# Kernel tuning notes

Measured on AMD Instinct MI355X. Metric: run time of the kernel, lower is better.

The kernel has to match this reference:

```python
import jax, jax.numpy as jnp
import numpy as np

N = 1024
IN_CH = 128
EDGE_CH = 32
OUT_CH = 128


def setup_inputs() -> dict:
    key = jax.random.key(0)
    ks = jax.random.split(key, 8)
    return {
        "node_mat": jax.random.normal(ks[0], (N, IN_CH), dtype=jnp.float32),
        "adj": jax.random.uniform(ks[1], (N, N), dtype=jnp.float32),
        "edge_adj": jax.random.uniform(ks[2], (EDGE_CH, N, N), dtype=jnp.float32),
        "node_weight": jax.random.normal(ks[3], (IN_CH, OUT_CH), dtype=jnp.float32) * 0.05,
        "edge_lay_1": jax.random.normal(ks[4], (EDGE_CH, OUT_CH - 1), dtype=jnp.float32) * 0.05,
        "edge_lay_2": jax.random.normal(ks[5], (OUT_CH - 1, OUT_CH), dtype=jnp.float32) * 0.05,
        "root": jax.random.normal(ks[6], (IN_CH, OUT_CH), dtype=jnp.float32) * 0.05,
        "bias": jax.random.normal(ks[7], (OUT_CH,), dtype=jnp.float32) * 0.05,
    }


def reference(node_mat, adj, edge_adj, node_weight, edge_lay_1, edge_lay_2, root, bias):
    # node message passing: adj-weighted sum of transformed node features  [N, out]
    sum_filter_node_msgs = adj @ (node_mat @ node_weight)
    # edge MLP: 2-layer with ReLU, applied over the edge-channel axis
    # edge_adj: [E, N, N]; edge_lay_1: [E, out-1] -> h1: [out-1, N, N]
    h1 = jnp.maximum(jnp.einsum('enm,eb->bnm', edge_adj, edge_lay_1), 0.0)
    # h1: [out-1, N, N]; edge_lay_2: [out-1, out] -> h2: [out, N, N]
    h2 = jnp.einsum('bnm,bo->onm', h1, edge_lay_2)
    # adjacency-weighted compression: e_compress[n, o] = sum_m h2[o, n, m] * adj[n, m]
    e_compress = jnp.einsum('onm,nm->no', h2, adj)
    root_info = node_mat @ root
    return sum_filter_node_msgs + e_compress + root_info + bias
```

## Files before the change

### kernel.cpp

```cpp
#include <hip/hip_runtime.h>
#include <hip/hip_bf16.h>

#define NN 1024
#define IN_CH 128
#define EDGE_CH 32
#define OUT_CH 128

typedef __attribute__((ext_vector_type(8))) short bf16x8;
typedef __attribute__((ext_vector_type(4))) float f32x4;

static __device__ __forceinline__ short f2bf(float f) {
    union { float f; unsigned u; } v; v.f = f;
    unsigned r = v.u + 0x7FFFu + ((v.u >> 16) & 1u);
    return (short)(r >> 16);
}

__global__ void node_gemm_kernel(const float* __restrict__ node_mat,
                                 const float* __restrict__ node_weight,
                                 const float* __restrict__ root,
                                 short* __restrict__ PT,
                                 float* __restrict__ R) {
    __shared__ float nm[2 * IN_CH];
    int tid = threadIdx.x;
    int n0 = blockIdx.x * 2;
    nm[tid] = node_mat[n0 * IN_CH + tid];
    __syncthreads();
    int o = tid & 127;
    int h = tid >> 7;
    const float* nr = &nm[h * IN_CH];
    float accp = 0.f, accr = 0.f;
#pragma unroll 8
    for (int c = 0; c < IN_CH; ++c) {
        float x = nr[c];
        accp += x * node_weight[c * OUT_CH + o];
        accr += x * root[c * OUT_CH + o];
    }
    R[(size_t)(n0 + h) * OUT_CH + o] = accr;
    PT[(size_t)o * NN + (n0 + h)] = f2bf(accp);
}

__global__ void edge_out_kernel(const float* __restrict__ edge_adj,
                                const float* __restrict__ adj,
                                const float* __restrict__ L1,
                                const float* __restrict__ L2,
                                const float* __restrict__ R,
                                const float* __restrict__ bias,
                                float* __restrict__ out) {
    int n = blockIdx.x;
    int tid = threadIdx.x;
    int wave = tid >> 6;
    int lane = tid & 63;
    int quad = lane >> 4;
    int col  = lane & 15;

    bf16x8 a_frag[8];
#pragma unroll
    for (int bt = 0; bt < 8; ++bt) {
        int b = bt * 16 + col;
#pragma unroll
        for (int j = 0; j < 8; ++j) {
            int e = quad * 8 + j;
            float v = (b < OUT_CH - 1) ? L1[e * (OUT_CH - 1) + b] : 0.0f;
            a_frag[bt][j] = f2bf(v);
        }
    }

    float g_acc[8][4];
#pragma unroll
    for (int bt = 0; bt < 8; ++bt)
#pragma unroll
        for (int r = 0; r < 4; ++r) g_acc[bt][r] = 0.0f;

    const float* adj_row = adj + (size_t)n * NN;
    const float* ea_base = edge_adj + (size_t)n * NN;

    for (int c = 0; c < 4; ++c) {
        int base = wave * 256 + c * 64;
        float adjv[4];
        bf16x8 bf[4];
#pragma unroll
        for (int s = 0; s < 4; ++s) {
            int m = base + s * 16 + col;
            adjv[s] = adj_row[m];
#pragma unroll
            for (int j = 0; j < 8; ++j) {
                size_t e = (size_t)(quad * 8 + j);
                bf[s][j] = f2bf(ea_base[e * (size_t)(NN * NN) + m]);
            }
        }
#pragma unroll
        for (int s = 0; s < 4; ++s) {
#pragma unroll
            for (int bt = 0; bt < 8; ++bt) {
                f32x4 d = __builtin_amdgcn_mfma_f32_16x16x32_bf16(
                    a_frag[bt], bf[s], (f32x4){0.f, 0.f, 0.f, 0.f}, 0, 0, 0);
#pragma unroll
                for (int r = 0; r < 4; ++r)
                    g_acc[bt][r] += fmaxf(d[r], 0.0f) * adjv[s];
            }
        }
    }

#pragma unroll
    for (int bt = 0; bt < 8; ++bt)
#pragma unroll
        for (int r = 0; r < 4; ++r) {
            float v = g_acc[bt][r];
            v += __shfl_xor(v, 1);
            v += __shfl_xor(v, 2);
            v += __shfl_xor(v, 4);
            v += __shfl_xor(v, 8);
            g_acc[bt][r] = v;
        }

    __shared__ float gred[4][OUT_CH];
    __shared__ float gs[OUT_CH];
    __shared__ float part[2][OUT_CH];
    if (col == 0) {
#pragma unroll
        for (int bt = 0; bt < 8; ++bt)
#pragma unroll
            for (int r = 0; r < 4; ++r)
                gred[wave][bt * 16 + quad * 4 + r] = g_acc[bt][r];
    }
    __syncthreads();
    if (tid < OUT_CH)
        gs[tid] = gred[0][tid] + gred[1][tid] + gred[2][tid] + gred[3][tid];
    __syncthreads();

    int o = tid & 127;
    int hf = tid >> 7;
    float acc = 0.f;
    int blo = hf * 64, bhi = hf ? 127 : 64;
#pragma unroll 8
    for (int b = blo; b < bhi; ++b)
        acc += gs[b] * L2[b * OUT_CH + o];
    part[hf][o] = acc;
    __syncthreads();
    if (tid < 128)
        out[(size_t)n * OUT_CH + tid] =
            part[0][tid] + part[1][tid] + R[(size_t)n * OUT_CH + tid] + bias[tid];
}

__global__ void adjp_kernel(const float* __restrict__ adj,
                            const short* __restrict__ PT,
                            float* __restrict__ out) {
    int blk = blockIdx.x;
    int nb = blk & 63;
    int oh = blk >> 6;
    int tid = threadIdx.x;
    int wave = tid >> 6;
    int lane = tid & 63;
    int quad = lane >> 4;
    int col  = lane & 15;
    int n0 = nb * 16;
    int o0 = oh * 64;

    f32x4 acc[4];
#pragma unroll
    for (int ot = 0; ot < 4; ++ot) acc[ot] = (f32x4){0.f, 0.f, 0.f, 0.f};

    int kbase = wave * 256;
#pragma unroll
    for (int ks = 0; ks < 8; ++ks) {
        int k = kbase + ks * 32 + quad * 8;
        const float* ap = adj + (size_t)(n0 + col) * NN + k;
        f32x4 a0 = *(const f32x4*)ap;
        f32x4 a1 = *(const f32x4*)(ap + 4);
        bf16x8 a;
#pragma unroll
        for (int j = 0; j < 4; ++j) { a[j] = f2bf(a0[j]); a[4 + j] = f2bf(a1[j]); }
#pragma unroll
        for (int ot = 0; ot < 4; ++ot) {
            int o = o0 + ot * 16 + col;
            bf16x8 b = *(const bf16x8*)(PT + (size_t)o * NN + k);
            acc[ot] = __builtin_amdgcn_mfma_f32_16x16x32_bf16(a, b, acc[ot], 0, 0, 0);
        }
    }

    __shared__ float red[4][16][65];
#pragma unroll
    for (int ot = 0; ot < 4; ++ot)
#pragma unroll
        for (int r = 0; r < 4; ++r)
            red[wave][quad * 4 + r][ot * 16 + col] = acc[ot][r];
    __syncthreads();

#pragma unroll
    for (int i = tid; i < 16 * 64; i += 256) {
        int rr = i >> 6;
        int cc = i & 63;
        float v = red[0][rr][cc] + red[1][rr][cc] + red[2][rr][cc] + red[3][rr][cc];
        out[(size_t)(n0 + rr) * OUT_CH + o0 + cc] += v;
    }
}

extern "C" void kernel_launch(void* const* d_in, const int* in_sizes, int n_in,
                              void* d_out, int out_size, void* d_ws, size_t ws_size,
                              hipStream_t stream) {
    const float* node_mat    = (const float*)d_in[0];
    const float* adj         = (const float*)d_in[1];
    const float* edge_adj    = (const float*)d_in[2];
    const float* node_weight = (const float*)d_in[3];
    const float* edge_lay_1  = (const float*)d_in[4];
    const float* edge_lay_2  = (const float*)d_in[5];
    const float* root        = (const float*)d_in[6];
    const float* bias        = (const float*)d_in[7];
    float* out = (float*)d_out;

    short* PT = (short*)d_ws;
    float* R  = (float*)((char*)d_ws + OUT_CH * NN * sizeof(short));

    node_gemm_kernel<<<NN / 2, 256, 0, stream>>>(node_mat, node_weight, root, PT, R);
    edge_out_kernel<<<NN, 256, 0, stream>>>(edge_adj, adj, edge_lay_1, edge_lay_2,
                                            R, bias, out);
    adjp_kernel<<<128, 256, 0, stream>>>(adj, PT, out);
}
```

Baseline: 243.9 us.

## Stage edge_adj tiles through double-buffered LDS with vectorized coalesced loads

```diff
diff --git a/kernel.cpp b/kernel.cpp
--- a/kernel.cpp
+++ b/kernel.cpp
@@ -53,6 +53,11 @@
     int quad = lane >> 4;
     int col  = lane & 15;
 
+    __shared__ short ea_lds[2][128 * 40];
+    __shared__ float gred[4][OUT_CH];
+    __shared__ float gs[OUT_CH];
+    __shared__ float part[2][OUT_CH];
+
     bf16x8 a_frag[8];
 #pragma unroll
     for (int bt = 0; bt < 8; ++bt) {
@@ -72,33 +77,55 @@
         for (int r = 0; r < 4; ++r) g_acc[bt][r] = 0.0f;
 
     const float* adj_row = adj + (size_t)n * NN;
-    const float* ea_base = edge_adj + (size_t)n * NN;
-
-    for (int c = 0; c < 4; ++c) {
-        int base = wave * 256 + c * 64;
-        float adjv[4];
-        bf16x8 bf[4];
-#pragma unroll
-        for (int s = 0; s < 4; ++s) {
-            int m = base + s * 16 + col;
-            adjv[s] = adj_row[m];
-#pragma unroll
-            for (int j = 0; j < 8; ++j) {
-                size_t e = (size_t)(quad * 8 + j);
-                bf[s][j] = f2bf(ea_base[e * (size_t)(NN * NN) + m]);
-            }
-        }
-#pragma unroll
-        for (int s = 0; s < 4; ++s) {
+
+    int se = tid >> 3;
+    int sm = (tid & 7) * 4;
+    const float* ea_row = edge_adj + (size_t)se * (size_t)(NN * NN) + (size_t)n * NN;
+
+    f32x4 st[4];
+#pragma unroll
+    for (int i = 0; i < 4; ++i)
+        st[i] = *(const f32x4*)(ea_row + sm + 32 * i);
+#pragma unroll
+    for (int i = 0; i < 4; ++i)
+#pragma unroll
+        for (int k = 0; k < 4; ++k)
+            ea_lds[0][(sm + 32 * i + k) * 40 + se] = f2bf(st[i][k]);
+    __syncthreads();
+
+    for (int c = 0; c < 8; ++c) {
+        int cur = c & 1;
+        if (c < 7) {
+            const float* p = ea_row + (c + 1) * 128;
+#pragma unroll
+            for (int i = 0; i < 4; ++i)
+                st[i] = *(const f32x4*)(p + sm + 32 * i);
+        }
+        int mloc0 = wave * 32;
+#pragma unroll
+        for (int s = 0; s < 2; ++s) {
+            int mloc = mloc0 + s * 16 + col;
+            float adjv = adj_row[c * 128 + mloc];
+            bf16x8 bf = *(const bf16x8*)((const char*)&ea_lds[cur][0] +
+                                         (size_t)mloc * 80 + quad * 16);
 #pragma unroll
             for (int bt = 0; bt < 8; ++bt) {
                 f32x4 d = __builtin_amdgcn_mfma_f32_16x16x32_bf16(
-                    a_frag[bt], bf[s], (f32x4){0.f, 0.f, 0.f, 0.f}, 0, 0, 0);
+                    a_frag[bt], bf, (f32x4){0.f, 0.f, 0.f, 0.f}, 0, 0, 0);
 #pragma unroll
                 for (int r = 0; r < 4; ++r)
-                    g_acc[bt][r] += fmaxf(d[r], 0.0f) * adjv[s];
+                    g_acc[bt][r] += fmaxf(d[r], 0.0f) * adjv;
             }
         }
+        if (c < 7) {
+            int nxt = cur ^ 1;
+#pragma unroll
+            for (int i = 0; i < 4; ++i)
+#pragma unroll
+                for (int k = 0; k < 4; ++k)
+                    ea_lds[nxt][(sm + 32 * i + k) * 40 + se] = f2bf(st[i][k]);
+        }
+        __syncthreads();
     }
 
 #pragma unroll
@@ -113,9 +140,6 @@
             g_acc[bt][r] = v;
         }
 
-    __shared__ float gred[4][OUT_CH];
-    __shared__ float gs[OUT_CH];
-    __shared__ float part[2][OUT_CH];
     if (col == 0) {
 #pragma unroll
         for (int bt = 0; bt < 8; ++bt)
```

After: 251.2 us. 3.0% more time.

## Stage edge_adj through LDS with coalesced vector loads, split rows across two blocks

Applied to the files above, without the earlier changes.

```diff
diff --git a/kernel.cpp b/kernel.cpp
--- a/kernel.cpp
+++ b/kernel.cpp
@@ -5,6 +5,7 @@
 #define IN_CH 128
 #define EDGE_CH 32
 #define OUT_CH 128
+#define NNSQ ((size_t)NN * (size_t)NN)
 
 typedef __attribute__((ext_vector_type(8))) short bf16x8;
 typedef __attribute__((ext_vector_type(4))) float f32x4;
@@ -39,111 +40,10 @@
     PT[(size_t)o * NN + (n0 + h)] = f2bf(accp);
 }
 
-__global__ void edge_out_kernel(const float* __restrict__ edge_adj,
-                                const float* __restrict__ adj,
-                                const float* __restrict__ L1,
-                                const float* __restrict__ L2,
-                                const float* __restrict__ R,
-                                const float* __restrict__ bias,
-                                float* __restrict__ out) {
-    int n = blockIdx.x;
-    int tid = threadIdx.x;
-    int wave = tid >> 6;
-    int lane = tid & 63;
-    int quad = lane >> 4;
-    int col  = lane & 15;
-
-    bf16x8 a_frag[8];
-#pragma unroll
-    for (int bt = 0; bt < 8; ++bt) {
-        int b = bt * 16 + col;
-#pragma unroll
-        for (int j = 0; j < 8; ++j) {
-            int e = quad * 8 + j;
-            float v = (b < OUT_CH - 1) ? L1[e * (OUT_CH - 1) + b] : 0.0f;
-            a_frag[bt][j] = f2bf(v);
-        }
-    }
-
-    float g_acc[8][4];
-#pragma unroll
-    for (int bt = 0; bt < 8; ++bt)
-#pragma unroll
-        for (int r = 0; r < 4; ++r) g_acc[bt][r] = 0.0f;
-
-    const float* adj_row = adj + (size_t)n * NN;
-    const float* ea_base = edge_adj + (size_t)n * NN;
-
-    for (int c = 0; c < 4; ++c) {
-        int base = wave * 256 + c * 64;
-        float adjv[4];
-        bf16x8 bf[4];
-#pragma unroll
-        for (int s = 0; s < 4; ++s) {
-            int m = base + s * 16 + col;
-            adjv[s] = adj_row[m];
-#pragma unroll
-            for (int j = 0; j < 8; ++j) {
-                size_t e = (size_t)(quad * 8 + j);
-                bf[s][j] = f2bf(ea_base[e * (size_t)(NN * NN) + m]);
-            }
-        }
-#pragma unroll
-        for (int s = 0; s < 4; ++s) {
-#pragma unroll
-            for (int bt = 0; bt < 8; ++bt) {
-                f32x4 d = __builtin_amdgcn_mfma_f32_16x16x32_bf16(
-                    a_frag[bt], bf[s], (f32x4){0.f, 0.f, 0.f, 0.f}, 0, 0, 0);
-#pragma unroll
-                for (int r = 0; r < 4; ++r)
-                    g_acc[bt][r] += fmaxf(d[r], 0.0f) * adjv[s];
-            }
-        }
-    }
-
-#pragma unroll
-    for (int bt = 0; bt < 8; ++bt)
-#pragma unroll
-        for (int r = 0; r < 4; ++r) {
-            float v = g_acc[bt][r];
-            v += __shfl_xor(v, 1);
-            v += __shfl_xor(v, 2);
-            v += __shfl_xor(v, 4);
-            v += __shfl_xor(v, 8);
-            g_acc[bt][r] = v;
-        }
-
-    __shared__ float gred[4][OUT_CH];
-    __shared__ float gs[OUT_CH];
-    __shared__ float part[2][OUT_CH];
-    if (col == 0) {
-#pragma unroll
-        for (int bt = 0; bt < 8; ++bt)
-#pragma unroll
-            for (int r = 0; r < 4; ++r)
-                gred[wave][bt * 16 + quad * 4 + r] = g_acc[bt][r];
-    }
-    __syncthreads();
-    if (tid < OUT_CH)
-        gs[tid] = gred[0][tid] + gred[1][tid] + gred[2][tid] + gred[3][tid];
-    __syncthreads();
-
-    int o = tid & 127;
-    int hf = tid >> 7;
-    float acc = 0.f;
-    int blo = hf * 64, bhi = hf ? 127 : 64;
-#pragma unroll 8
-    for (int b = blo; b < bhi; ++b)
-        acc += gs[b] * L2[b * OUT_CH + o];
-    part[hf][o] = acc;
-    __syncthreads();
-    if (tid < 128)
-        out[(size_t)n * OUT_CH + tid] =
-            part[0][tid] + part[1][tid] + R[(size_t)n * OUT_CH + tid] + bias[tid];
-}
-
 __global__ void adjp_kernel(const float* __restrict__ adj,
                             const short* __restrict__ PT,
+                            const float* __restrict__ R,
+                            const float* __restrict__ bias,
                             float* __restrict__ out) {
     int blk = blockIdx.x;
     int nb = blk & 63;
@@ -191,8 +91,133 @@
         int rr = i >> 6;
         int cc = i & 63;
         float v = red[0][rr][cc] + red[1][rr][cc] + red[2][rr][cc] + red[3][rr][cc];
-        out[(size_t)(n0 + rr) * OUT_CH + o0 + cc] += v;
-    }
+        size_t idx = (size_t)(n0 + rr) * OUT_CH + o0 + cc;
+        out[idx] = v + R[idx] + bias[o0 + cc];
+    }
+}
+
+__global__ void edge_out_kernel(const float* __restrict__ edge_adj,
+                                const float* __restrict__ adj,
+                                const float* __restrict__ L1,
+                                const float* __restrict__ L2,
+                                float* __restrict__ out) {
+    int n    = blockIdx.x >> 1;
+    int half = blockIdx.x & 1;
+    int tid = threadIdx.x;
+    int wave = tid >> 6;
+    int lane = tid & 63;
+    int quad = lane >> 4;
+    int col  = lane & 15;
+
+    __shared__ __attribute__((aligned(16))) short ea_lds[2][64 * 40];
+    __shared__ float gred[4][OUT_CH];
+    __shared__ float gs[OUT_CH];
+    __shared__ float part[2][OUT_CH];
+
+    bf16x8 a_frag[8];
+#pragma unroll
+    for (int bt = 0; bt < 8; ++bt) {
+        int b = bt * 16 + col;
+#pragma unroll
+        for (int j = 0; j < 8; ++j) {
+            int e = quad * 8 + j;
+            float v = (b < OUT_CH - 1) ? L1[e * (OUT_CH - 1) + b] : 0.0f;
+            a_frag[bt][j] = f2bf(v);
+        }
+    }
+
+    float g_acc[8][4];
+#pragma unroll
+    for (int bt = 0; bt < 8; ++bt)
+#pragma unroll
+        for (int r = 0; r < 4; ++r) g_acc[bt][r] = 0.0f;
+
+    int mbase = half * 512;
+    const float* adj_row = adj + (size_t)n * NN + mbase;
+
+    int se = tid >> 3;
+    int sm = (tid & 7) * 4;
+    const float* ea_t = edge_adj + (size_t)se * NNSQ + (size_t)n * NN + mbase + sm;
+
+    short* buf0 = &ea_lds[0][0];
+    short* buf1 = &ea_lds[1][0];
+
+    f32x4 stA0, stA1, stB0, stB1;
+
+#define LOAD_A(CH) { stA0 = *(const f32x4*)(ea_t + (CH) * 64); \
+                     stA1 = *(const f32x4*)(ea_t + (CH) * 64 + 32); }
+#define LOAD_B(CH) { stB0 = *(const f32x4*)(ea_t + (CH) * 64); \
+                     stB1 = *(const f32x4*)(ea_t + (CH) * 64 + 32); }
+#define CONVERT(S0, S1, BUF) { \
+        _Pragma("unroll") for (int k = 0; k < 4; ++k) { \
+            (BUF)[(sm + k) * 40 + se]      = f2bf((S0)[k]); \
+            (BUF)[(sm + 32 + k) * 40 + se] = f2bf((S1)[k]); } }
+#define COMPUTE(BUF, CH) { \
+        int mloc = wave * 16 + col; \
+        float adjv = adj_row[(CH) * 64 + mloc]; \
+        bf16x8 bfv = *(const bf16x8*)((BUF) + mloc * 40 + quad * 8); \
+        _Pragma("unroll") for (int bt = 0; bt < 8; ++bt) { \
+            f32x4 d = __builtin_amdgcn_mfma_f32_16x16x32_bf16( \
+                a_frag[bt], bfv, (f32x4){0.f, 0.f, 0.f, 0.f}, 0, 0, 0); \
+            _Pragma("unroll") for (int r = 0; r < 4; ++r) \
+                g_acc[bt][r] += fmaxf(d[r], 0.0f) * adjv; } }
+
+    LOAD_A(0);
+    LOAD_B(1);
+    CONVERT(stA0, stA1, buf0);
+    __syncthreads();
+
+    for (int cc = 0; cc < 4; ++cc) {
+        int c0 = cc * 2;
+        if (c0 + 2 < 8) LOAD_A(c0 + 2);
+        COMPUTE(buf0, c0);
+        CONVERT(stB0, stB1, buf1);
+        __syncthreads();
+        if (c0 + 3 < 8) LOAD_B(c0 + 3);
+        COMPUTE(buf1, c0 + 1);
+        if (c0 + 2 < 8) CONVERT(stA0, stA1, buf0);
+        __syncthreads();
+    }
+#undef LOAD_A
+#undef LOAD_B
+#undef CONVERT
+#undef COMPUTE
+
+#pragma unroll
+    for (int bt = 0; bt < 8; ++bt)
+#pragma unroll
+        for (int r = 0; r < 4; ++r) {
+            float v = g_acc[bt][r];
+            v += __shfl_xor(v, 1);
+            v += __shfl_xor(v, 2);
+            v += __shfl_xor(v, 4);
+            v += __shfl_xor(v, 8);
+            g_acc[bt][r] = v;
+        }
+
+    if (col == 0) {
+#pragma unroll
+        for (int bt = 0; bt < 8; ++bt)
+#pragma unroll
+            for (int r = 0; r < 4; ++r)
+                gred[wave][bt * 16 + quad * 4 + r] = g_acc[bt][r];
+    }
+    __syncthreads();
+    if (tid < OUT_CH)
+        gs[tid] = gred[0][tid] + gred[1][tid] + gred[2][tid] + gred[3][tid];
+    __syncthreads();
+
+    int o = tid & 127;
+    int hf = tid >> 7;
+    float acc = 0.f;
+    int blo = hf * 64, bhi = hf ? 127 : 64;
+#pragma unroll 8
+    for (int b = blo; b < bhi; ++b)
+        acc += gs[b] * L2[b * OUT_CH + o];
+    part[hf][o] = acc;
+    __syncthreads();
+    if (tid < 128)
+        atomicAdd(&out[(size_t)n * OUT_CH + tid], part[0][tid] + part[1][tid]);
 }
 
 extern "C" void kernel_launch(void* const* d_in, const int* in_sizes, int n_in,
@@ -212,7 +237,7 @@
     float* R  = (float*)((char*)d_ws + OUT_CH * NN * sizeof(short));
 
     node_gemm_kernel<<<NN / 2, 256, 0, stream>>>(node_mat, node_weight, root, PT, R);
-    edge_out_kernel<<<NN, 256, 0, stream>>>(edge_adj, adj, edge_lay_1, edge_lay_2,
-                                            R, bias, out);
-    adjp_kernel<<<128, 256, 0, stream>>>(adj, PT, out);
-}
+    adjp_kernel<<<128, 256, 0, stream>>>(adj, PT, R, bias, out);
+    edge_out_kernel<<<2 * NN, 256, 0, stream>>>(edge_adj, adj, edge_lay_1,
+                                                edge_lay_2, out);
+}
```

Result: slower. 391.3 us (+60.5%).

## Stage edge_adj through double-buffered LDS with vectorized loads and split output channels

Applied to the files above, without the earlier changes.

```diff
diff --git a/kernel.cpp b/kernel.cpp
--- a/kernel.cpp
+++ b/kernel.cpp
@@ -5,6 +5,7 @@
 #define IN_CH 128
 #define EDGE_CH 32
 #define OUT_CH 128
+#define NNSQ ((size_t)NN * (size_t)NN)
 
 typedef __attribute__((ext_vector_type(8))) short bf16x8;
 typedef __attribute__((ext_vector_type(4))) float f32x4;
@@ -39,111 +40,10 @@
     PT[(size_t)o * NN + (n0 + h)] = f2bf(accp);
 }
 
-__global__ void edge_out_kernel(const float* __restrict__ edge_adj,
-                                const float* __restrict__ adj,
-                                const float* __restrict__ L1,
-                                const float* __restrict__ L2,
-                                const float* __restrict__ R,
-                                const float* __restrict__ bias,
-                                float* __restrict__ out) {
-    int n = blockIdx.x;
-    int tid = threadIdx.x;
-    int wave = tid >> 6;
-    int lane = tid & 63;
-    int quad = lane >> 4;
-    int col  = lane & 15;
-
-    bf16x8 a_frag[8];
-#pragma unroll
-    for (int bt = 0; bt < 8; ++bt) {
-        int b = bt * 16 + col;
-#pragma unroll
-        for (int j = 0; j < 8; ++j) {
-            int e = quad * 8 + j;
-            float v = (b < OUT_CH - 1) ? L1[e * (OUT_CH - 1) + b] : 0.0f;
-            a_frag[bt][j] = f2bf(v);
-        }
-    }
-
-    float g_acc[8][4];
-#pragma unroll
-    for (int bt = 0; bt < 8; ++bt)
-#pragma unroll
-        for (int r = 0; r < 4; ++r) g_acc[bt][r] = 0.0f;
-
-    const float* adj_row = adj + (size_t)n * NN;
-    const float* ea_base = edge_adj + (size_t)n * NN;
-
-    for (int c = 0; c < 4; ++c) {
-        int base = wave * 256 + c * 64;
-        float adjv[4];
-        bf16x8 bf[4];
-#pragma unroll
-        for (int s = 0; s < 4; ++s) {
-            int m = base + s * 16 + col;
-            adjv[s] = adj_row[m];
-#pragma unroll
-            for (int j = 0; j < 8; ++j) {
-                size_t e = (size_t)(quad * 8 + j);
-                bf[s][j] = f2bf(ea_base[e * (size_t)(NN * NN) + m]);
-            }
-        }
-#pragma unroll
-        for (int s = 0; s < 4; ++s) {
-#pragma unroll
-            for (int bt = 0; bt < 8; ++bt) {
-                f32x4 d = __builtin_amdgcn_mfma_f32_16x16x32_bf16(
-                    a_frag[bt], bf[s], (f32x4){0.f, 0.f, 0.f, 0.f}, 0, 0, 0);
-#pragma unroll
-                for (int r = 0; r < 4; ++r)
-                    g_acc[bt][r] += fmaxf(d[r], 0.0f) * adjv[s];
-            }
-        }
-    }
-
-#pragma unroll
-    for (int bt = 0; bt < 8; ++bt)
-#pragma unroll
-        for (int r = 0; r < 4; ++r) {
-            float v = g_acc[bt][r];
-            v += __shfl_xor(v, 1);
-            v += __shfl_xor(v, 2);
-            v += __shfl_xor(v, 4);
-            v += __shfl_xor(v, 8);
-            g_acc[bt][r] = v;
-        }
-
-    __shared__ float gred[4][OUT_CH];
-    __shared__ float gs[OUT_CH];
-    __shared__ float part[2][OUT_CH];
-    if (col == 0) {
-#pragma unroll
-        for (int bt = 0; bt < 8; ++bt)
-#pragma unroll
-            for (int r = 0; r < 4; ++r)
-                gred[wave][bt * 16 + quad * 4 + r] = g_acc[bt][r];
-    }
-    __syncthreads();
-    if (tid < OUT_CH)
-        gs[tid] = gred[0][tid] + gred[1][tid] + gred[2][tid] + gred[3][tid];
-    __syncthreads();
-
-    int o = tid & 127;
-    int hf = tid >> 7;
-    float acc = 0.f;
-    int blo = hf * 64, bhi = hf ? 127 : 64;
-#pragma unroll 8
-    for (int b = blo; b < bhi; ++b)
-        acc += gs[b] * L2[b * OUT_CH + o];
-    part[hf][o] = acc;
-    __syncthreads();
-    if (tid < 128)
-        out[(size_t)n * OUT_CH + tid] =
-            part[0][tid] + part[1][tid] + R[(size_t)n * OUT_CH + tid] + bias[tid];
-}
-
 __global__ void adjp_kernel(const float* __restrict__ adj,
                             const short* __restrict__ PT,
+                            const float* __restrict__ R,
+                            const float* __restrict__ bias,
                             float* __restrict__ out) {
     int blk = blockIdx.x;
     int nb = blk & 63;
@@ -191,7 +91,122 @@
         int rr = i >> 6;
         int cc = i & 63;
         float v = red[0][rr][cc] + red[1][rr][cc] + red[2][rr][cc] + red[3][rr][cc];
-        out[(size_t)(n0 + rr) * OUT_CH + o0 + cc] += v;
+        size_t idx = (size_t)(n0 + rr) * OUT_CH + o0 + cc;
+        out[idx] = v + R[idx] + bias[o0 + cc];
+    }
+}
+
+__global__ void edge_out_kernel(const float* __restrict__ edge_adj,
+                                const float* __restrict__ adj,
+                                const float* __restrict__ L1,
+                                const float* __restrict__ L2,
+                                float* __restrict__ out) {
+    int n = blockIdx.x;
+    int tid = threadIdx.x;
+    int wave = tid >> 6;
+    int lane = tid & 63;
+    int quad = lane >> 4;
+    int col  = lane & 15;
+
+    __shared__ __attribute__((aligned(16))) short ea_lds[2][256 * 40];
+    __shared__ float adj_lds[NN];
+    __shared__ float gs[OUT_CH];
+    __shared__ float part[2][OUT_CH];
+
+    *(f32x4*)&adj_lds[tid * 4] = *(const f32x4*)(adj + (size_t)n * NN + tid * 4);
+
+    bf16x8 a_frag0, a_frag1;
+#pragma unroll
+    for (int j = 0; j < 8; ++j) {
+        int e = quad * 8 + j;
+        int b0 = (wave * 2 + 0) * 16 + col;
+        int b1 = (wave * 2 + 1) * 16 + col;
+        a_frag0[j] = f2bf((b0 < OUT_CH - 1) ? L1[e * (OUT_CH - 1) + b0] : 0.0f);
+        a_frag1[j] = f2bf((b1 < OUT_CH - 1) ? L1[e * (OUT_CH - 1) + b1] : 0.0f);
+    }
+
+    float g0[4] = {0.f, 0.f, 0.f, 0.f};
+    float g1[4] = {0.f, 0.f, 0.f, 0.f};
+
+    const float* ea_b = edge_adj + (size_t)(wave * 8) * NNSQ + (size_t)n * NN + lane * 4;
+
+    f32x4 st0, st1, st2, st3, st4, st5, st6, st7;
+
+#define ISSUE(AC) { \
+        const float* p_ = ea_b + (AC) * 256; \
+        st0 = *(const f32x4*)(p_ + 0 * NNSQ); st1 = *(const f32x4*)(p_ + 1 * NNSQ); \
+        st2 = *(const f32x4*)(p_ + 2 * NNSQ); st3 = *(const f32x4*)(p_ + 3 * NNSQ); \
+        st4 = *(const f32x4*)(p_ + 4 * NNSQ); st5 = *(const f32x4*)(p_ + 5 * NNSQ); \
+        st6 = *(const f32x4*)(p_ + 6 * NNSQ); st7 = *(const f32x4*)(p_ + 7 * NNSQ); }
+#define CONVERT(BUF) { \
+        _Pragma("unroll") for (int k = 0; k < 4; ++k) { \
+            bf16x8 pk_; \
+            pk_[0] = f2bf(st0[k]); pk_[1] = f2bf(st1[k]); \
+            pk_[2] = f2bf(st2[k]); pk_[3] = f2bf(st3[k]); \
+            pk_[4] = f2bf(st4[k]); pk_[5] = f2bf(st5[k]); \
+            pk_[6] = f2bf(st6[k]); pk_[7] = f2bf(st7[k]); \
+            *(bf16x8*)((BUF) + (lane * 4 + k) * 40 + wave * 8) = pk_; } }
+#define COMPUTE(BUF, AC) { \
+        _Pragma("unroll") for (int st = 0; st < 16; ++st) { \
+            int mrow = st * 16 + col; \
+            float adjv = adj_lds[(AC) * 256 + mrow]; \
+            bf16x8 bfv = *(const bf16x8*)((BUF) + mrow * 40 + quad * 8); \
+            f32x4 d0 = __builtin_amdgcn_mfma_f32_16x16x32_bf16( \
+                a_frag0, bfv, (f32x4){0.f, 0.f, 0.f, 0.f}, 0, 0, 0); \
+            f32x4 d1 = __builtin_amdgcn_mfma_f32_16x16x32_bf16( \
+                a_frag1, bfv, (f32x4){0.f, 0.f, 0.f, 0.f}, 0, 0, 0); \
+            _Pragma("unroll") for (int r = 0; r < 4; ++r) { \
+                g0[r] += fmaxf(d0[r], 0.0f) * adjv; \
+                g1[r] += fmaxf(d1[r], 0.0f) * adjv; } } }
+
+    ISSUE(n & 3);
+    CONVERT(&ea_lds[0][0]);
+    __syncthreads();
+
+#pragma unroll
+    for (int c = 0; c < 4; ++c) {
+        short* bufc = &ea_lds[c & 1][0];
+        short* bufn = &ea_lds[(c & 1) ^ 1][0];
+        if (c < 3) ISSUE((n + c + 1) & 3);
+        COMPUTE(bufc, (n + c) & 3);
+        if (c < 3) CONVERT(bufn);
+        __syncthreads();
+    }
+#undef ISSUE
+#undef CONVERT
+#undef COMPUTE
+
+#pragma unroll
+    for (int r = 0; r < 4; ++r) {
+        float v0 = g0[r], v1 = g1[r];
+        v0 += __shfl_xor(v0, 1); v1 += __shfl_xor(v1, 1);
+        v0 += __shfl_xor(v0, 2); v1 += __shfl_xor(v1, 2);
+        v0 += __shfl_xor(v0, 4); v1 += __shfl_xor(v1, 4);
+        v0 += __shfl_xor(v0, 8); v1 += __shfl_xor(v1, 8);
+        g0[r] = v0; g1[r] = v1;
+    }
+
+    if (col == 0) {
+#pragma unroll
+        for (int r = 0; r < 4; ++r) {
+            gs[(wave * 2 + 0) * 16 + quad * 4 + r] = g0[r];
+            gs[(wave * 2 + 1) * 16 + quad * 4 + r] = g1[r];
+        }
+    }
+    __syncthreads();
+
+    int o = tid & 127;
+    int hf = tid >> 7;
+    float acc = 0.f;
+    int blo = hf * 64, bhi = hf ? 127 : 64;
+#pragma unroll 8
+    for (int b = blo; b < bhi; ++b)
+        acc += gs[b] * L2[b * OUT_CH + o];
+    part[hf][o] = acc;
+    __syncthreads();
+    if (tid < 128) {
+        size_t idx = (size_t)n * OUT_CH + tid;
+        out[idx] += part[0][tid] + part[1][tid];
     }
 }
 
@@ -212,7 +227,7 @@
     float* R  = (float*)((char*)d_ws + OUT_CH * NN * sizeof(short));
 
     node_gemm_kernel<<<NN / 2, 256, 0, stream>>>(node_mat, node_weight, root, PT, R);
-    edge_out_kernel<<<NN, 256, 0, stream>>>(edge_adj, adj, edge_lay_1, edge_lay_2,
-                                            R, bias, out);
-    adjp_kernel<<<128, 256, 0, stream>>>(adj, PT, out);
-}
+    adjp_kernel<<<128, 256, 0, stream>>>(adj, PT, R, bias, out);
+    edge_out_kernel<<<NN, 256, 0, stream>>>(edge_adj, adj, edge_lay_1,
+                                            edge_lay_2, out);
+}
```

After: 274.0 us. 12.3% more time.
